# Optimization experiments

Measured on AMD Instinct MI355X. Metric: run time of the kernel, lower is better.

Reference implementation:

```python
import jax, jax.numpy as jnp
import numpy as np

B, L, I, H, D, T = 4096, 128, 64, 256, 32, 101


def setup_inputs() -> dict:
    key = jax.random.key(0)
    ks = jax.random.split(key, 8)
    def w(k, shape, fan):
        return (jax.random.uniform(k, shape, jnp.float32) * 2.0 - 1.0) / np.sqrt(fan).astype(np.float32)
    return {
        "ts": jnp.arange(T, dtype=jnp.float32) * 0.01,              # [T] uniform grid, dt = 0.01
        "y0": jax.random.normal(ks[0], (B, D), jnp.float32),
        "input_seq": jax.random.normal(ks[1], (B, L, I), jnp.float32),
        "dW": jax.random.normal(ks[2], (T - 1, B, D), jnp.float32),  # standard normal; scaled by sqrt(dt) inside
        "W_ih": w(ks[3], (4 * H, I), H),
        "W_hh": w(ks[4], (4 * H, H), H),
        "b_ih": jnp.zeros((4 * H,), jnp.float32),
        "b_hh": jnp.zeros((4 * H,), jnp.float32),
        "drift_W": w(ks[5], (D, H + D), H + D),
        "drift_b": jnp.zeros((D,), jnp.float32),
        "diff_W": w(ks[6], (D, H + D), H + D),
        "diff_b": jnp.zeros((D,), jnp.float32),
    }


def _lstm_last_hidden(x, W_ih, W_hh, b_ih, b_hh):
    # x: [B, L, I]; returns final hidden state h_L: [B, H]. PyTorch gate order: i, f, g, o.
    b = b_ih + b_hh
    Hh = W_hh.shape[1]
    x_proj = jnp.einsum('bli,gi->lbg', x, W_ih) + b  # [L, B, 4H] precompute input projections

    def step(carry, xp):
        h, c = carry
        gates = xp + h @ W_hh.T
        i, f, g, o = jnp.split(gates, 4, axis=1)
        c = jax.nn.sigmoid(f) * c + jax.nn.sigmoid(i) * jnp.tanh(g)
        h = jax.nn.sigmoid(o) * jnp.tanh(c)
        return (h, c), None

    h0 = jnp.zeros((x.shape[0], Hh), x.dtype)
    (h, _), _ = jax.lax.scan(step, (h0, h0), x_proj)
    return h


def reference(ts, y0, input_seq, dW, W_ih, W_hh, b_ih, b_hh, drift_W, drift_b, diff_W, diff_b):
    # Encoder: drift_lstm final hidden state, hidden.squeeze(0) -> [B, H]
    hid = _lstm_last_hidden(input_seq, W_ih, W_hh, b_ih, b_hh)
    dts = ts[1:] - ts[:-1]  # [T-1], each equal to solver dt (0.01)

    def euler_step(y, inp):
        dt, dw = inp
        comb = jnp.concatenate([hid, y], axis=1)          # [B, H+D]
        f = comb @ drift_W.T + drift_b                    # drift
        g = comb @ diff_W.T + diff_b                      # diagonal diffusion
        y_next = y + f * dt + g * (dw * jnp.sqrt(dt))     # Euler-Maruyama, dW ~ N(0, dt)
        return y_next, y_next

    _, ys = jax.lax.scan(euler_step, y0, (dts, dW))
    return jnp.concatenate([y0[None], ys], axis=0)        # [T, B, D], like torchsde.sdeint
```

## Files before the change

### kernel.cpp

```cpp
#include <hip/hip_runtime.h>
#include <hip/hip_bf16.h>
#include <stdint.h>

#define B_ 4096
#define L_ 128
#define I_ 64
#define H_ 256
#define D_ 32
#define T_ 101
#define K_ 320
#define NG 1024

typedef __attribute__((ext_vector_type(8))) short short8;
typedef __attribute__((ext_vector_type(4))) float f32x4;

__device__ __forceinline__ void gload16(const void* g, const void* l) {
  __builtin_amdgcn_global_load_lds(
      (const __attribute__((address_space(1))) void*)(uintptr_t)g,
      (__attribute__((address_space(3))) void*)(uintptr_t)l, 16, 0, 0);
}

__device__ __forceinline__ float sigf(float x) { return 1.0f / (1.0f + __expf(-x)); }
__device__ __forceinline__ float tanhf_(float x) { return 2.0f / (1.0f + __expf(-2.0f * x)) - 1.0f; }

__global__ void prep_w(const float* __restrict__ W_ih, const float* __restrict__ W_hh,
                       const float* __restrict__ b_ih, const float* __restrict__ b_hh,
                       __hip_bfloat16* __restrict__ Wc, float* __restrict__ bc) {
  int idx = blockIdx.x * 256 + threadIdx.x;
  if (idx < NG * K_) {
    int n = idx / K_, k = idx % K_;
    int g = (n >> 4) & 3;
    int u = (n & 15) | ((n >> 6) << 4);
    int r = g * H_ + u;
    float v = (k < I_) ? W_ih[r * I_ + k] : W_hh[r * H_ + (k - I_)];
    Wc[idx] = __float2bfloat16(v);
  }
  if (idx < NG) {
    int n = idx;
    int g = (n >> 4) & 3;
    int u = (n & 15) | ((n >> 6) << 4);
    int r = g * H_ + u;
    bc[n] = b_ih[r] + b_hh[r];
  }
}

__global__ void prep_x(const float* __restrict__ x, __hip_bfloat16* __restrict__ xT) {
  int l = blockIdx.x;
  int b = blockIdx.y * 4 + threadIdx.y;
  int i = threadIdx.x;
  xT[((size_t)l * B_ + b) * I_ + i] = __float2bfloat16(x[((size_t)b * L_ + l) * I_ + i]);
}

__global__ void prep_zero(__hip_bfloat16* __restrict__ h0, float* __restrict__ c) {
  int idx = blockIdx.x * 256 + threadIdx.x;
  if (idx < B_ * H_) {
    h0[idx] = __float2bfloat16(0.0f);
    c[idx] = 0.0f;
  }
}

__global__ __launch_bounds__(512) void lstm_step2(
    const __hip_bfloat16* __restrict__ x_t,
    const __hip_bfloat16* __restrict__ h_in,
    __hip_bfloat16* __restrict__ h_out,
    const __hip_bfloat16* __restrict__ Wc,
    const float* __restrict__ bc,
    float* __restrict__ c)
{
  __shared__ __hip_bfloat16 As[2][128 * 64];
  __shared__ __hip_bfloat16 Bs[2][128 * 64];

  const int tid = threadIdx.x;
  const int lane = tid & 63;
  const int wid = tid >> 6;
  const int wm = wid & 3;
  const int wn = wid >> 2;

  const int flat = blockIdx.x;
  const int xcd = flat & 7, slot = flat >> 3;
  const int b_idx = xcd * 4 + (slot >> 3);
  const int n_idx = slot & 7;
  const int b0 = b_idx * 128, n0 = n_idx * 128;

  const int colb = lane & 15;

  f32x4 acc[2][4];
  #pragma unroll
  for (int ni = 0; ni < 4; ++ni) {
    const float bv = bc[n0 + wn * 64 + ni * 16 + colb];
    #pragma unroll
    for (int mi = 0; mi < 2; ++mi)
      #pragma unroll
      for (int j = 0; j < 4; ++j) acc[mi][ni][j] = bv;
  }

  const int sr8 = lane >> 3;
  const int sch = lane & 7;
  const int srcch = sch ^ sr8;

  #define STAGE(kk, buf)                                                             \
    {                                                                                \
      _Pragma("unroll")                                                              \
      for (int c2 = 0; c2 < 2; ++c2) {                                               \
        const int r = (c2 * 8 + wid) * 8 + sr8;                                      \
        const char* srcA;                                                            \
        if ((kk) == 0)                                                               \
          srcA = (const char*)x_t + (((size_t)(b0 + r)) * I_ + srcch * 8) * 2;       \
        else                                                                         \
          srcA = (const char*)h_in +                                                 \
                 (((size_t)(b0 + r)) * H_ + ((kk)*64 - 64) + srcch * 8) * 2;         \
        gload16(srcA, (const char*)As[buf] + (c2 * 8 + wid) * 1024);                 \
        const char* srcB = (const char*)Wc +                                         \
                           (((size_t)(n0 + r)) * K_ + (kk)*64 + srcch * 8) * 2;      \
        gload16(srcB, (const char*)Bs[buf] + (c2 * 8 + wid) * 1024);                 \
      }                                                                              \
    }

  STAGE(0, 0);
  __syncthreads();

  #pragma unroll
  for (int kk = 0; kk < 5; ++kk) {
    const int cur = kk & 1;
    if (kk < 4) STAGE(kk + 1, cur ^ 1);

    const char* Ab = (const char*)As[cur];
    const char* Bb = (const char*)Bs[cur];
    short8 av[2][2], bv[2][4];
    #pragma unroll
    for (int ks = 0; ks < 2; ++ks) {
      const int cc = ks * 4 + (lane >> 4);
      #pragma unroll
      for (int mi = 0; mi < 2; ++mi) {
        const int rr = wm * 32 + mi * 16 + colb;
        av[ks][mi] = *(const short8*)(Ab + rr * 128 + (cc ^ (rr & 7)) * 16);
      }
      #pragma unroll
      for (int ni = 0; ni < 4; ++ni) {
        const int rr = wn * 64 + ni * 16 + colb;
        bv[ks][ni] = *(const short8*)(Bb + rr * 128 + (cc ^ (rr & 7)) * 16);
      }
    }
    #pragma unroll
    for (int ks = 0; ks < 2; ++ks)
      #pragma unroll
      for (int mi = 0; mi < 2; ++mi)
        #pragma unroll
        for (int ni = 0; ni < 4; ++ni)
          acc[mi][ni] =
              __builtin_amdgcn_mfma_f32_16x16x32_bf16(av[ks][mi], bv[ks][ni], acc[mi][ni], 0, 0, 0);
    __syncthreads();
  }

  const int u = 32 * n_idx + 16 * wn + colb;
  #pragma unroll
  for (int mi = 0; mi < 2; ++mi) {
    #pragma unroll
    for (int r = 0; r < 4; ++r) {
      const int row = b0 + wm * 32 + mi * 16 + (lane >> 4) * 4 + r;
      const float iv = sigf(acc[mi][0][r]);
      const float fv = sigf(acc[mi][1][r]);
      const float gv = tanhf_(acc[mi][2][r]);
      const float ov = sigf(acc[mi][3][r]);
      float cc = c[(size_t)row * H_ + u];
      cc = fv * cc + iv * gv;
      c[(size_t)row * H_ + u] = cc;
      h_out[(size_t)row * H_ + u] = __float2bfloat16(ov * tanhf_(cc));
    }
  }
  #undef STAGE
}

__global__ __launch_bounds__(256) void hid_proj(
    const __hip_bfloat16* __restrict__ h, const float* __restrict__ drift_W,
    const float* __restrict__ drift_b, const float* __restrict__ diff_W,
    const float* __restrict__ diff_b, float* __restrict__ fhid, float* __restrict__ ghid) {
  __shared__ float WdL[H_ * D_];
  __shared__ float WgL[H_ * D_];
  for (int idx = threadIdx.x; idx < H_ * D_; idx += 256) {
    int k = idx >> 5, d = idx & 31;
    WdL[idx] = drift_W[d * (H_ + D_) + k];
    WgL[idx] = diff_W[d * (H_ + D_) + k];
  }
  __syncthreads();
  const int row = blockIdx.x * 8 + (threadIdx.x >> 5);
  const int d = threadIdx.x & 31;
  const __hip_bfloat16* hr = h + (size_t)row * H_;
  float f = drift_b[d], g = diff_b[d];
  for (int k = 0; k < H_; ++k) {
    float hv = __bfloat162float(hr[k]);
    f += hv * WdL[k * 32 + d];
    g += hv * WgL[k * 32 + d];
  }
  fhid[(size_t)row * D_ + d] = f;
  ghid[(size_t)row * D_ + d] = g;
}

__global__ __launch_bounds__(256) void sde_kernel(
    const float* __restrict__ ts, const float* __restrict__ y0, const float* __restrict__ dW,
    const float* __restrict__ drift_W, const float* __restrict__ diff_W,
    const float* __restrict__ fhid, const float* __restrict__ ghid, float* __restrict__ out) {
  const int g = blockIdx.x * 256 + threadIdx.x;
  const int d = g & 31;
  float A[32], G[32];
  #pragma unroll
  for (int k = 0; k < 32; ++k) {
    A[k] = drift_W[d * (H_ + D_) + H_ + k];
    G[k] = diff_W[d * (H_ + D_) + H_ + k];
  }
  float y = y0[g];
  const float fh = fhid[g], gh = ghid[g];
  out[g] = y;
  float dw0 = dW[g];
  float dw1 = dW[(size_t)(B_ * D_) + g];
  for (int t = 0; t < T_ - 1; ++t) {
    float dwn = 0.0f;
    if (t + 2 < T_ - 1) dwn = dW[(size_t)(t + 2) * (B_ * D_) + g];
    const float dt = ts[t + 1] - ts[t];
    const float sdt = sqrtf(dt);
    float f0 = 0.f, f1 = 0.f, f2 = 0.f, f3 = 0.f;
    float g0 = 0.f, g1 = 0.f, g2 = 0.f, g3 = 0.f;
    #pragma unroll
    for (int kq = 0; kq < 8; ++kq) {
      const float y0v = __shfl(y, kq * 4 + 0, 32);
      const float y1v = __shfl(y, kq * 4 + 1, 32);
      const float y2v = __shfl(y, kq * 4 + 2, 32);
      const float y3v = __shfl(y, kq * 4 + 3, 32);
      f0 += A[kq * 4 + 0] * y0v; g0 += G[kq * 4 + 0] * y0v;
      f1 += A[kq * 4 + 1] * y1v; g1 += G[kq * 4 + 1] * y1v;
      f2 += A[kq * 4 + 2] * y2v; g2 += G[kq * 4 + 2] * y2v;
      f3 += A[kq * 4 + 3] * y3v; g3 += G[kq * 4 + 3] * y3v;
    }
    const float f = fh + ((f0 + f1) + (f2 + f3));
    const float gg = gh + ((g0 + g1) + (g2 + g3));
    y = y + f * dt + gg * (dw0 * sdt);
    out[(size_t)(t + 1) * (B_ * D_) + g] = y;
    dw0 = dw1;
    dw1 = dwn;
  }
}

extern "C" void kernel_launch(void* const* d_in, const int* in_sizes, int n_in,
                              void* d_out, int out_size, void* d_ws, size_t ws_size,
                              hipStream_t stream) {
  const float* ts = (const float*)d_in[0];
  const float* y0 = (const float*)d_in[1];
  const float* xseq = (const float*)d_in[2];
  const float* dW = (const float*)d_in[3];
  const float* W_ih = (const float*)d_in[4];
  const float* W_hh = (const float*)d_in[5];
  const float* b_ih = (const float*)d_in[6];
  const float* b_hh = (const float*)d_in[7];
  const float* drift_W = (const float*)d_in[8];
  const float* drift_b = (const float*)d_in[9];
  const float* diff_W = (const float*)d_in[10];
  const float* diff_b = (const float*)d_in[11];
  float* out = (float*)d_out;

  char* p = (char*)d_ws;
  __hip_bfloat16* xT = (__hip_bfloat16*)p; p += (size_t)L_ * B_ * I_ * 2;
  __hip_bfloat16* Wc = (__hip_bfloat16*)p; p += (size_t)NG * K_ * 2;
  float* bc = (float*)p;                   p += (size_t)NG * 4;
  __hip_bfloat16* h0 = (__hip_bfloat16*)p; p += (size_t)B_ * H_ * 2;
  __hip_bfloat16* h1 = (__hip_bfloat16*)p; p += (size_t)B_ * H_ * 2;
  float* c = (float*)p;                    p += (size_t)B_ * H_ * 4;
  float* fh = (float*)p;                   p += (size_t)B_ * D_ * 4;
  float* gh = (float*)p;                   p += (size_t)B_ * D_ * 4;

  prep_w<<<(NG * K_ + 255) / 256, 256, 0, stream>>>(W_ih, W_hh, b_ih, b_hh, Wc, bc);
  prep_x<<<dim3(L_, B_ / 4), dim3(64, 4), 0, stream>>>(xseq, xT);
  prep_zero<<<(B_ * H_ + 255) / 256, 256, 0, stream>>>(h0, c);

  __hip_bfloat16* hb[2] = {h0, h1};
  for (int t = 0; t < L_; ++t) {
    lstm_step2<<<256, 512, 0, stream>>>(xT + (size_t)t * B_ * I_, hb[t & 1],
                                        hb[(t + 1) & 1], Wc, bc, c);
  }
  hid_proj<<<B_ / 8, 256, 0, stream>>>(hb[L_ & 1], drift_W, drift_b, diff_W, diff_b, fh, gh);
  sde_kernel<<<(B_ * D_) / 256, 256, 0, stream>>>(ts, y0, dW, drift_W, diff_W, fh, gh, out);
}
```

Baseline: 1.321 ms.

## Fuse LSTM timesteps into persistent cooperative kernel with per-batch-tile barriers

Replaces 128 separate per-timestep LSTM launches with one cooperative persistent kernel that loops over time. The cell state stays in registers, and the 8 blocks sharing a batch tile synchronise through an atomic counter barrier, so there is no launch overhead and no global c traffic per step. The SDE kernel also switches from shuffles to an LDS broadcast of y. This risks spin-wait cost, and it relies on all 256 blocks being co-resident, which the cooperative launch is meant to ensure.

```diff
diff --git a/kernel.cpp b/kernel.cpp
--- a/kernel.cpp
+++ b/kernel.cpp
@@ -51,21 +51,19 @@
   xT[((size_t)l * B_ + b) * I_ + i] = __float2bfloat16(x[((size_t)b * L_ + l) * I_ + i]);
 }
 
-__global__ void prep_zero(__hip_bfloat16* __restrict__ h0, float* __restrict__ c) {
+__global__ void prep_zero(__hip_bfloat16* __restrict__ hA, unsigned int* __restrict__ barct) {
   int idx = blockIdx.x * 256 + threadIdx.x;
-  if (idx < B_ * H_) {
-    h0[idx] = __float2bfloat16(0.0f);
-    c[idx] = 0.0f;
-  }
-}
-
-__global__ __launch_bounds__(512) void lstm_step2(
-    const __hip_bfloat16* __restrict__ x_t,
-    const __hip_bfloat16* __restrict__ h_in,
-    __hip_bfloat16* __restrict__ h_out,
+  if (idx < B_ * H_) hA[idx] = __float2bfloat16(0.0f);
+  if (idx < 32) barct[idx] = 0u;
+}
+
+__global__ __launch_bounds__(512, 2) void lstm_persist(
+    const __hip_bfloat16* __restrict__ xT,
+    __hip_bfloat16* __restrict__ hA,
+    __hip_bfloat16* __restrict__ hB,
     const __hip_bfloat16* __restrict__ Wc,
     const float* __restrict__ bc,
-    float* __restrict__ c)
+    unsigned int* __restrict__ barct)
 {
   __shared__ __hip_bfloat16 As[2][128 * 64];
   __shared__ __hip_bfloat16 Bs[2][128 * 64];
@@ -81,33 +79,34 @@
   const int b_idx = xcd * 4 + (slot >> 3);
   const int n_idx = slot & 7;
   const int b0 = b_idx * 128, n0 = n_idx * 128;
-
   const int colb = lane & 15;
 
-  f32x4 acc[2][4];
+  float bv4[4];
   #pragma unroll
-  for (int ni = 0; ni < 4; ++ni) {
-    const float bv = bc[n0 + wn * 64 + ni * 16 + colb];
-    #pragma unroll
-    for (int mi = 0; mi < 2; ++mi)
-      #pragma unroll
-      for (int j = 0; j < 4; ++j) acc[mi][ni][j] = bv;
-  }
+  for (int ni = 0; ni < 4; ++ni) bv4[ni] = bc[n0 + wn * 64 + ni * 16 + colb];
+
+  float creg[2][4];
+  #pragma unroll
+  for (int mi = 0; mi < 2; ++mi)
+    #pragma unroll
+    for (int r = 0; r < 4; ++r) creg[mi][r] = 0.0f;
 
   const int sr8 = lane >> 3;
   const int sch = lane & 7;
   const int srcch = sch ^ sr8;
 
-  #define STAGE(kk, buf)                                                             \
+  const int u = 32 * n_idx + 16 * wn + colb;
+
+  #define STAGE(kk, buf, xt, hin)                                                    \
     {                                                                                \
       _Pragma("unroll")                                                              \
       for (int c2 = 0; c2 < 2; ++c2) {                                               \
         const int r = (c2 * 8 + wid) * 8 + sr8;                                      \
         const char* srcA;                                                            \
         if ((kk) == 0)                                                               \
-          srcA = (const char*)x_t + (((size_t)(b0 + r)) * I_ + srcch * 8) * 2;       \
+          srcA = (const char*)(xt) + (((size_t)(b0 + r)) * I_ + srcch * 8) * 2;      \
         else                                                                         \
-          srcA = (const char*)h_in +                                                 \
+          srcA = (const char*)(hin) +                                                \
                  (((size_t)(b0 + r)) * H_ + ((kk)*64 - 64) + srcch * 8) * 2;         \
         gload16(srcA, (const char*)As[buf] + (c2 * 8 + wid) * 1024);                 \
         const char* srcB = (const char*)Wc +                                         \
@@ -116,57 +115,80 @@
       }                                                                              \
     }
 
-  STAGE(0, 0);
-  __syncthreads();
-
-  #pragma unroll
-  for (int kk = 0; kk < 5; ++kk) {
-    const int cur = kk & 1;
-    if (kk < 4) STAGE(kk + 1, cur ^ 1);
-
-    const char* Ab = (const char*)As[cur];
-    const char* Bb = (const char*)Bs[cur];
-    short8 av[2][2], bv[2][4];
-    #pragma unroll
-    for (int ks = 0; ks < 2; ++ks) {
-      const int cc = ks * 4 + (lane >> 4);
-      #pragma unroll
-      for (int mi = 0; mi < 2; ++mi) {
-        const int rr = wm * 32 + mi * 16 + colb;
-        av[ks][mi] = *(const short8*)(Ab + rr * 128 + (cc ^ (rr & 7)) * 16);
-      }
-      #pragma unroll
-      for (int ni = 0; ni < 4; ++ni) {
-        const int rr = wn * 64 + ni * 16 + colb;
-        bv[ks][ni] = *(const short8*)(Bb + rr * 128 + (cc ^ (rr & 7)) * 16);
-      }
-    }
-    #pragma unroll
-    for (int ks = 0; ks < 2; ++ks)
+  for (int t = 0; t < L_; ++t) {
+    const __hip_bfloat16* hin = (t & 1) ? hB : hA;
+    __hip_bfloat16* hout = (t & 1) ? hA : hB;
+    const __hip_bfloat16* xt = xT + (size_t)t * B_ * I_;
+
+    f32x4 acc[2][4];
+    #pragma unroll
+    for (int ni = 0; ni < 4; ++ni)
       #pragma unroll
       for (int mi = 0; mi < 2; ++mi)
         #pragma unroll
-        for (int ni = 0; ni < 4; ++ni)
-          acc[mi][ni] =
-              __builtin_amdgcn_mfma_f32_16x16x32_bf16(av[ks][mi], bv[ks][ni], acc[mi][ni], 0, 0, 0);
+        for (int j = 0; j < 4; ++j) acc[mi][ni][j] = bv4[ni];
+
+    STAGE(0, 0, xt, hin);
     __syncthreads();
-  }
-
-  const int u = 32 * n_idx + 16 * wn + colb;
-  #pragma unroll
-  for (int mi = 0; mi < 2; ++mi) {
-    #pragma unroll
-    for (int r = 0; r < 4; ++r) {
-      const int row = b0 + wm * 32 + mi * 16 + (lane >> 4) * 4 + r;
-      const float iv = sigf(acc[mi][0][r]);
-      const float fv = sigf(acc[mi][1][r]);
-      const float gv = tanhf_(acc[mi][2][r]);
-      const float ov = sigf(acc[mi][3][r]);
-      float cc = c[(size_t)row * H_ + u];
-      cc = fv * cc + iv * gv;
-      c[(size_t)row * H_ + u] = cc;
-      h_out[(size_t)row * H_ + u] = __float2bfloat16(ov * tanhf_(cc));
-    }
+
+    #pragma unroll
+    for (int kk = 0; kk < 5; ++kk) {
+      const int cur = kk & 1;
+      if (kk < 4) STAGE(kk + 1, cur ^ 1, xt, hin);
+
+      const char* Ab = (const char*)As[cur];
+      const char* Bb = (const char*)Bs[cur];
+      short8 av[2][2], bv[2][4];
+      #pragma unroll
+      for (int ks = 0; ks < 2; ++ks) {
+        const int cc = ks * 4 + (lane >> 4);
+        #pragma unroll
+        for (int mi = 0; mi < 2; ++mi) {
+          const int rr = wm * 32 + mi * 16 + colb;
+          av[ks][mi] = *(const short8*)(Ab + rr * 128 + (cc ^ (rr & 7)) * 16);
+        }
+        #pragma unroll
+        for (int ni = 0; ni < 4; ++ni) {
+          const int rr = wn * 64 + ni * 16 + colb;
+          bv[ks][ni] = *(const short8*)(Bb + rr * 128 + (cc ^ (rr & 7)) * 16);
+        }
+      }
+      #pragma unroll
+      for (int ks = 0; ks < 2; ++ks)
+        #pragma unroll
+        for (int mi = 0; mi < 2; ++mi)
+          #pragma unroll
+          for (int ni = 0; ni < 4; ++ni)
+            acc[mi][ni] = __builtin_amdgcn_mfma_f32_16x16x32_bf16(av[ks][mi], bv[ks][ni],
+                                                                  acc[mi][ni], 0, 0, 0);
+      __syncthreads();
+    }
+
+    #pragma unroll
+    for (int mi = 0; mi < 2; ++mi) {
+      #pragma unroll
+      for (int r = 0; r < 4; ++r) {
+        const int row = b0 + wm * 32 + mi * 16 + (lane >> 4) * 4 + r;
+        const float iv = sigf(acc[mi][0][r]);
+        const float fv = sigf(acc[mi][1][r]);
+        const float gv = tanhf_(acc[mi][2][r]);
+        const float ov = sigf(acc[mi][3][r]);
+        float cc = fv * creg[mi][r] + iv * gv;
+        creg[mi][r] = cc;
+        hout[(size_t)row * H_ + u] = __float2bfloat16(ov * tanhf_(cc));
+      }
+    }
+
+    __syncthreads();
+    if (tid == 0) {
+      __hip_atomic_fetch_add(barct + b_idx, 1u, __ATOMIC_RELEASE, __HIP_MEMORY_SCOPE_AGENT);
+      const unsigned int target = 8u * (unsigned int)(t + 1);
+      while (__hip_atomic_load(barct + b_idx, __ATOMIC_ACQUIRE, __HIP_MEMORY_SCOPE_AGENT) <
+             target) {
+        __builtin_amdgcn_s_sleep(2);
+      }
+    }
+    __syncthreads();
   }
   #undef STAGE
 }
@@ -200,8 +222,11 @@
     const float* __restrict__ ts, const float* __restrict__ y0, const float* __restrict__ dW,
     const float* __restrict__ drift_W, const float* __restrict__ diff_W,
     const float* __restrict__ fhid, const float* __restrict__ ghid, float* __restrict__ out) {
-  const int g = blockIdx.x * 256 + threadIdx.x;
+  __shared__ float ylds[256];
+  const int tid = threadIdx.x;
+  const int g = blockIdx.x * 256 + tid;
   const int d = g & 31;
+  const int rb = tid & ~31;
   float A[32], G[32];
   #pragma unroll
   for (int k = 0; k < 32; ++k) {
@@ -218,18 +243,16 @@
     if (t + 2 < T_ - 1) dwn = dW[(size_t)(t + 2) * (B_ * D_) + g];
     const float dt = ts[t + 1] - ts[t];
     const float sdt = sqrtf(dt);
+    ylds[tid] = y;
     float f0 = 0.f, f1 = 0.f, f2 = 0.f, f3 = 0.f;
     float g0 = 0.f, g1 = 0.f, g2 = 0.f, g3 = 0.f;
     #pragma unroll
-    for (int kq = 0; kq < 8; ++kq) {
-      const float y0v = __shfl(y, kq * 4 + 0, 32);
-      const float y1v = __shfl(y, kq * 4 + 1, 32);
-      const float y2v = __shfl(y, kq * 4 + 2, 32);
-      const float y3v = __shfl(y, kq * 4 + 3, 32);
-      f0 += A[kq * 4 + 0] * y0v; g0 += G[kq * 4 + 0] * y0v;
-      f1 += A[kq * 4 + 1] * y1v; g1 += G[kq * 4 + 1] * y1v;
-      f2 += A[kq * 4 + 2] * y2v; g2 += G[kq * 4 + 2] * y2v;
-      f3 += A[kq * 4 + 3] * y3v; g3 += G[kq * 4 + 3] * y3v;
+    for (int c = 0; c < 8; ++c) {
+      const f32x4 yv = *(const f32x4*)&ylds[rb + c * 4];
+      f0 += A[c * 4 + 0] * yv[0]; g0 += G[c * 4 + 0] * yv[0];
+      f1 += A[c * 4 + 1] * yv[1]; g1 += G[c * 4 + 1] * yv[1];
+      f2 += A[c * 4 + 2] * yv[2]; g2 += G[c * 4 + 2] * yv[2];
+      f3 += A[c * 4 + 3] * yv[3]; g3 += G[c * 4 + 3] * yv[3];
     }
     const float f = fh + ((f0 + f1) + (f2 + f3));
     const float gg = gh + ((g0 + g1) + (g2 + g3));
@@ -261,21 +284,26 @@
   __hip_bfloat16* xT = (__hip_bfloat16*)p; p += (size_t)L_ * B_ * I_ * 2;
   __hip_bfloat16* Wc = (__hip_bfloat16*)p; p += (size_t)NG * K_ * 2;
   float* bc = (float*)p;                   p += (size_t)NG * 4;
-  __hip_bfloat16* h0 = (__hip_bfloat16*)p; p += (size_t)B_ * H_ * 2;
-  __hip_bfloat16* h1 = (__hip_bfloat16*)p; p += (size_t)B_ * H_ * 2;
-  float* c = (float*)p;                    p += (size_t)B_ * H_ * 4;
+  __hip_bfloat16* hA = (__hip_bfloat16*)p; p += (size_t)B_ * H_ * 2;
+  __hip_bfloat16* hB = (__hip_bfloat16*)p; p += (size_t)B_ * H_ * 2;
   float* fh = (float*)p;                   p += (size_t)B_ * D_ * 4;
   float* gh = (float*)p;                   p += (size_t)B_ * D_ * 4;
+  unsigned int* barct = (unsigned int*)p;  p += 32 * 4;
 
   prep_w<<<(NG * K_ + 255) / 256, 256, 0, stream>>>(W_ih, W_hh, b_ih, b_hh, Wc, bc);
   prep_x<<<dim3(L_, B_ / 4), dim3(64, 4), 0, stream>>>(xseq, xT);
-  prep_zero<<<(B_ * H_ + 255) / 256, 256, 0, stream>>>(h0, c);
-
-  __hip_bfloat16* hb[2] = {h0, h1};
-  for (int t = 0; t < L_; ++t) {
-    lstm_step2<<<256, 512, 0, stream>>>(xT + (size_t)t * B_ * I_, hb[t & 1],
-                                        hb[(t + 1) & 1], Wc, bc, c);
-  }
-  hid_proj<<<B_ / 8, 256, 0, stream>>>(hb[L_ & 1], drift_W, drift_b, diff_W, diff_b, fh, gh);
+  prep_zero<<<(B_ * H_ + 255) / 256, 256, 0, stream>>>(hA, barct);
+
+  {
+    const __hip_bfloat16* xT_c = xT;
+    const __hip_bfloat16* Wc_c = Wc;
+    const float* bc_c = bc;
+    void* args[] = {(void*)&xT_c, (void*)&hA, (void*)&hB, (void*)&Wc_c, (void*)&bc_c,
+                    (void*)&barct};
+    hipLaunchCooperativeKernel(reinterpret_cast<void*>(lstm_persist), dim3(256), dim3(512),
+                               args, 0, stream);
+  }
+
+  hid_proj<<<B_ / 8, 256, 0, stream>>>(hA, drift_W, drift_b, diff_W, diff_b, fh, gh);
   sde_kernel<<<(B_ * D_) / 256, 256, 0, stream>>>(ts, y0, dW, drift_W, diff_W, fh, gh, out);
 }
```

New measurement: 2.435 ms. +84.3%, slower.
